# Kernel tuning notes

Hardware: AMD Instinct MI355X
Metric: run time of the kernel (lower is better)

Reference implementation:

```python
import jax, jax.numpy as jnp
import numpy as np

B, S, D = 2, 2048, 2048
H, KVH, HD = 8, 1, 256          # query heads, kv heads, head_dim (GQA: n_rep = H // KVH)
ROPE_THETA = 10000.0
NEG_INF = -1e9


def setup_inputs() -> dict:
    key = jax.random.key(0)
    k1, k2, k3, k4, k5 = jax.random.split(key, 5)
    hidden_states = jax.random.normal(k1, (B, S, D), dtype=jnp.float32)
    # additive causal mask: 0 where allowed, -inf where masked, shape (B,1,S,S)
    causal = jnp.tril(jnp.ones((S, S), dtype=bool))
    attention_mask = jnp.where(causal, 0.0, NEG_INF).astype(jnp.float32)
    attention_mask = jnp.broadcast_to(attention_mask[None, None], (B, 1, S, S))
    position_ids = jnp.broadcast_to(jnp.arange(S, dtype=jnp.int32)[None, :], (B, S))
    sc = 0.02
    Wq = jax.random.normal(k2, (H * HD, D), dtype=jnp.float32) * sc   # torch Linear weight layout [out,in]
    Wk = jax.random.normal(k3, (KVH * HD, D), dtype=jnp.float32) * sc
    Wv = jax.random.normal(k4, (KVH * HD, D), dtype=jnp.float32) * sc
    Wo = jax.random.normal(k5, (D, H * HD), dtype=jnp.float32) * sc
    return {"hidden_states": hidden_states, "attention_mask": attention_mask,
            "position_ids": position_ids, "Wq": Wq, "Wk": Wk, "Wv": Wv, "Wo": Wo}


def _rotate_half(x):
    x1, x2 = jnp.split(x, 2, axis=-1)
    return jnp.concatenate((-x2, x1), axis=-1)


def _rope_cos_sin(position_ids):
    inv_freq = 1.0 / (ROPE_THETA ** (jnp.arange(0, HD, 2, dtype=jnp.float32) / HD))  # [HD/2]
    freqs = position_ids.astype(jnp.float32)[:, :, None] * inv_freq[None, None, :]   # [B,S,HD/2]
    emb = jnp.concatenate((freqs, freqs), axis=-1)                                   # [B,S,HD]
    return jnp.cos(emb)[:, None], jnp.sin(emb)[:, None]                              # [B,1,S,HD]


def reference(hidden_states, attention_mask, position_ids, Wq, Wk, Wv, Wo):
    q = (hidden_states @ Wq.T).reshape(B, S, H, HD).transpose(0, 2, 1, 3)     # [B,H,S,HD]
    k = (hidden_states @ Wk.T).reshape(B, S, KVH, HD).transpose(0, 2, 1, 3)   # [B,KVH,S,HD]
    v = (hidden_states @ Wv.T).reshape(B, S, KVH, HD).transpose(0, 2, 1, 3)
    cos, sin = _rope_cos_sin(position_ids)
    q = q * cos + _rotate_half(q) * sin
    k = k * cos + _rotate_half(k) * sin
    n_rep = H // KVH
    k = jnp.repeat(k, n_rep, axis=1)                                          # repeat_kv -> [B,H,S,HD]
    v = jnp.repeat(v, n_rep, axis=1)
    scores = jnp.einsum('bhqd,bhkd->bhqk', q, k) / jnp.sqrt(jnp.float32(HD))
    scores = scores + attention_mask
    attn = jax.nn.softmax(scores, axis=-1)                                    # dropout p=0 (eval)
    ctx = jnp.einsum('bhqk,bhkd->bhqd', attn, v)
    ctx = ctx.transpose(0, 2, 1, 3).reshape(B, S, H * HD)
    out = ctx @ Wo.T
    return out, attn
```

## Files before the change

### kernel.cpp

```cpp
#include <hip/hip_runtime.h>
#include <hip/hip_bf16.h>
#include <math.h>

typedef __bf16 bf16_t;
typedef __bf16 bf16x8 __attribute__((ext_vector_type(8)));
typedef __bf16 bf16x4 __attribute__((ext_vector_type(4)));
typedef float  f32x4  __attribute__((ext_vector_type(4)));

#define DEV __device__ __forceinline__

constexpr int B_   = 2;
constexpr int S_   = 2048;
constexpr int D_   = 2048;
constexpr int H_   = 8;
constexpr int HD_  = 256;
constexpr int NQKV_ = H_ * HD_ + 2 * HD_;
constexpr int TOK_ = B_ * S_;

#if defined(__has_builtin)
#if __has_builtin(__builtin_amdgcn_global_load_lds)
#define HAS_GLLDS 1
#endif
#endif

DEV void stage16(const bf16_t* g, bf16_t* l) {
#ifdef HAS_GLLDS
  __builtin_amdgcn_global_load_lds((const __attribute__((address_space(1))) void*)g,
                                   (__attribute__((address_space(3))) void*)l, 16, 0, 0);
#else
  *(bf16x8*)l = *(const bf16x8*)g;
#endif
}

__global__ void cast_inputs(const float* __restrict__ hs, const float* __restrict__ wq,
                            const float* __restrict__ wk, const float* __restrict__ wv,
                            const float* __restrict__ wo,
                            bf16_t* __restrict__ Xb, bf16_t* __restrict__ Wqkvb,
                            bf16_t* __restrict__ Wob) {
  const size_t i = (size_t)blockIdx.x * blockDim.x + threadIdx.x;
  const size_t NHS = (size_t)TOK_ * D_;
  const size_t NWQ = (size_t)H_ * HD_ * D_;
  const size_t NWK = (size_t)HD_ * D_;
  if (i < NHS) Xb[i] = (bf16_t)hs[i];
  if (i < NWQ) { Wqkvb[i] = (bf16_t)wq[i]; Wob[i] = (bf16_t)wo[i]; }
  if (i < NWK) { Wqkvb[NWQ + i] = (bf16_t)wk[i]; Wqkvb[NWQ + NWK + i] = (bf16_t)wv[i]; }
}

template <int MODE>
__global__ __launch_bounds__(256, 2)
void gemm_bt(const void* __restrict__ Av, const bf16_t* __restrict__ Bg0,
             void* __restrict__ Cv,
             int M, int N, int K, int lda, int ldb, int ldc, float scale)
{
  const int bn = blockIdx.x, bm = blockIdx.y, z = blockIdx.z;
  if (MODE == 1 && bn > bm) return;

  const int m0 = bm * 128, n0 = bn * 128;
  const bf16_t* Ab = nullptr;
  const float*  Af = nullptr;
  const bf16_t* Bg = Bg0;
  if (MODE == 0) { Ab = (const bf16_t*)Av; }
  if (MODE == 1) { Ab = (const bf16_t*)Av + (size_t)z * S_ * HD_; Bg += (size_t)(z >> 3) * S_ * HD_; }
  if (MODE == 2) { Af = (const float*)Av + (size_t)z * S_ * S_;   Bg += (size_t)(z >> 3) * HD_ * S_; }

  int kend = K;
  if (MODE == 2) { int kl = (bm + 1) * 128; kend = kl < K ? kl : K; }

  __shared__ __align__(16) bf16_t Asm[128 * 32];
  __shared__ __align__(16) bf16_t Bsm[128 * 32];

  const int tid  = threadIdx.x;
  const int l    = tid & 63;
  const int w    = tid >> 6;
  const int wm   = (w >> 1) * 64;
  const int wn   = (w & 1) * 64;
  const int lrow = l & 15;
  const int quad = l >> 4;

  f32x4 acc[4][4] = {};

  for (int k0 = 0; k0 < kend; k0 += 32) {
    __syncthreads();
    if (MODE != 2) {
      #pragma unroll
      for (int c = 0; c < 2; ++c) {
        int chunk = c * 256 + tid;
        int row = chunk >> 2, col = (chunk & 3) << 3;
        stage16(Ab + (size_t)(m0 + row) * lda + (k0 + col), &Asm[row * 32 + col]);
      }
    } else {
      #pragma unroll
      for (int c = 0; c < 4; ++c) {
        int chunk = c * 256 + tid;
        int row = chunk >> 3, col = (chunk & 7) << 2;
        float4 v = *(const float4*)(Af + (size_t)(m0 + row) * lda + (k0 + col));
        bf16x4 t; t[0] = (bf16_t)v.x; t[1] = (bf16_t)v.y; t[2] = (bf16_t)v.z; t[3] = (bf16_t)v.w;
        *(bf16x4*)&Asm[row * 32 + col] = t;
      }
    }
    #pragma unroll
    for (int c = 0; c < 2; ++c) {
      int chunk = c * 256 + tid;
      int row = chunk >> 2, col = (chunk & 3) << 3;
      stage16(Bg + (size_t)(n0 + row) * ldb + (k0 + col), &Bsm[row * 32 + col]);
    }
    __syncthreads();

    bf16x8 af[4], bfr[4];
    #pragma unroll
    for (int i = 0; i < 4; ++i)
      af[i] = *(const bf16x8*)&Asm[(wm + i * 16 + lrow) * 32 + quad * 8];
    #pragma unroll
    for (int j = 0; j < 4; ++j)
      bfr[j] = *(const bf16x8*)&Bsm[(wn + j * 16 + lrow) * 32 + quad * 8];
    #pragma unroll
    for (int i = 0; i < 4; ++i)
      #pragma unroll
      for (int j = 0; j < 4; ++j)
        acc[i][j] = __builtin_amdgcn_mfma_f32_16x16x32_bf16(af[i], bfr[j], acc[i][j], 0, 0, 0);
  }

  if (MODE == 2) {
    bf16_t* C = (bf16_t*)Cv + (size_t)(z >> 3) * S_ * D_ + (size_t)(z & 7) * HD_;
    #pragma unroll
    for (int i = 0; i < 4; ++i) {
      int row = wm + i * 16 + quad * 4;
      #pragma unroll
      for (int j = 0; j < 4; ++j) {
        int col = n0 + wn + j * 16 + lrow;
        #pragma unroll
        for (int r = 0; r < 4; ++r)
          C[(size_t)(m0 + row + r) * ldc + col] = (bf16_t)(acc[i][j][r] * scale);
      }
    }
  } else {
    float* C = (float*)Cv;
    if (MODE == 1) C += (size_t)z * S_ * S_;
    #pragma unroll
    for (int i = 0; i < 4; ++i) {
      int row = wm + i * 16 + quad * 4;
      #pragma unroll
      for (int j = 0; j < 4; ++j) {
        int col = n0 + wn + j * 16 + lrow;
        #pragma unroll
        for (int r = 0; r < 4; ++r)
          C[(size_t)(m0 + row + r) * ldc + col] = acc[i][j][r] * scale;
      }
    }
  }
}

__global__ void rope_kernel(const float* __restrict__ qkv, const int* __restrict__ pos_ids,
                            bf16_t* __restrict__ Qh, bf16_t* __restrict__ Kb,
                            bf16_t* __restrict__ Vt)
{
  const int t = blockIdx.x;
  const int b = t >> 11, s = t & (S_ - 1);
  const int tid = threadIdx.x;
  const int pd = tid & 127, half = tid >> 7;
  const float pos = (float)pos_ids[t];
  const float expo = (float)(2 * pd) * (1.0f / 256.0f);
  const float invf = 1.0f / powf(10000.0f, expo);
  const float ang = pos * invf;
  const float c = cosf(ang), sn = sinf(ang);
  const float* base = qkv + (size_t)t * NQKV_;
  const int other = half ? tid - 128 : tid + 128;
  const float sgn = half ? 1.0f : -1.0f;
  #pragma unroll
  for (int h = 0; h < H_; ++h) {
    float x = base[h * HD_ + tid];
    float xo = base[h * HD_ + other];
    Qh[((size_t)(b * H_ + h) * S_ + s) * HD_ + tid] = (bf16_t)(x * c + sgn * xo * sn);
  }
  {
    float x = base[D_ + tid], xo = base[D_ + other];
    Kb[(size_t)t * HD_ + tid] = (bf16_t)(x * c + sgn * xo * sn);
  }
  {
    float x = base[D_ + HD_ + tid];
    Vt[((size_t)b * HD_ + tid) * S_ + s] = (bf16_t)x;
  }
}

__global__ __launch_bounds__(256)
void softmax_rows(float* __restrict__ attn)
{
  const int r = blockIdx.x;
  const int q = r & (S_ - 1);
  float* row = attn + (size_t)r * S_;
  const int tid = threadIdx.x;
  __shared__ float red[8];
  float vals[8];
  float mx = -3.0e38f;
  #pragma unroll
  for (int i = 0; i < 8; ++i) {
    int c = i * 256 + tid;
    float v = row[c];
    vals[i] = v;
    if (c <= q) mx = fmaxf(mx, v);
  }
  #pragma unroll
  for (int o = 32; o > 0; o >>= 1) mx = fmaxf(mx, __shfl_xor(mx, o, 64));
  if ((tid & 63) == 0) red[tid >> 6] = mx;
  __syncthreads();
  mx = fmaxf(fmaxf(red[0], red[1]), fmaxf(red[2], red[3]));
  float sum = 0.f;
  #pragma unroll
  for (int i = 0; i < 8; ++i) {
    int c = i * 256 + tid;
    if (c <= q) { vals[i] = __expf(vals[i] - mx); sum += vals[i]; }
    else vals[i] = 0.f;
  }
  #pragma unroll
  for (int o = 32; o > 0; o >>= 1) sum += __shfl_xor(sum, o, 64);
  if ((tid & 63) == 0) red[4 + (tid >> 6)] = sum;
  __syncthreads();
  sum = (red[4] + red[5]) + (red[6] + red[7]);
  const float inv = 1.0f / sum;
  #pragma unroll
  for (int i = 0; i < 8; ++i) {
    int c = i * 256 + tid;
    row[c] = vals[i] * inv;
  }
}

extern "C" void kernel_launch(void* const* d_in, const int* in_sizes, int n_in,
                              void* d_out, int out_size, void* d_ws, size_t ws_size,
                              hipStream_t stream)
{
  const float* hs  = (const float*)d_in[0];
  const int*   pos = (const int*)d_in[2];
  const float* wq  = (const float*)d_in[3];
  const float* wk  = (const float*)d_in[4];
  const float* wv  = (const float*)d_in[5];
  const float* wo  = (const float*)d_in[6];

  float* out  = (float*)d_out;
  float* attn = out + (size_t)TOK_ * D_;

  char* ws = (char*)d_ws;
  bf16_t* Xb    = (bf16_t*)(ws);
  bf16_t* Wqkvb = (bf16_t*)(ws + 16777216);
  bf16_t* Wob   = (bf16_t*)(ws + 27262976);
  float*  QKV   = (float* )(ws + 35651584);
  bf16_t* Ctx   = (bf16_t*)(ws + 35651584);
  bf16_t* Qh    = (bf16_t*)(ws + 77594624);
  bf16_t* Kb    = (bf16_t*)(ws + 94371840);
  bf16_t* Vt    = (bf16_t*)(ws + 96468992);

  cast_inputs<<<(TOK_ * D_) / 256, 256, 0, stream>>>(hs, wq, wk, wv, wo, Xb, Wqkvb, Wob);
  gemm_bt<0><<<dim3(NQKV_ / 128, TOK_ / 128, 1), 256, 0, stream>>>(
      Xb, Wqkvb, QKV, TOK_, NQKV_, D_, D_, D_, NQKV_, 1.0f);
  rope_kernel<<<TOK_, 256, 0, stream>>>(QKV, pos, Qh, Kb, Vt);
  gemm_bt<1><<<dim3(S_ / 128, S_ / 128, B_ * H_), 256, 0, stream>>>(
      Qh, Kb, attn, S_, S_, HD_, HD_, HD_, S_, 0.0625f);
  softmax_rows<<<B_ * H_ * S_, 256, 0, stream>>>(attn);
  gemm_bt<2><<<dim3(HD_ / 128, S_ / 128, B_ * H_), 256, 0, stream>>>(
      attn, Vt, Ctx, S_, HD_, S_, S_, S_, D_, 1.0f);
  gemm_bt<0><<<dim3(D_ / 128, TOK_ / 128, 1), 256, 0, stream>>>(
      Ctx, Wob, out, TOK_, D_, D_, D_, D_, D_, 1.0f);
}
```

Before: 678.5 us.

## Fuse QK^T, softmax and PV into a two-pass flash-attention kernel

Replaces the separate score GEMM, row softmax and PV GEMM with a single flash-attention kernel. A first pass computes running row max and sum, and a second pass recomputes the scores, writes normalized probabilities to attn (zeros above the diagonal), and accumulates P·V from a bf16 copy in shared memory. The goal is to avoid reading and rewriting the full fp32 attn matrix several times. The QKV projection now writes bf16 instead of fp32, which halves the intermediate traffic at some precision cost. QK^T is computed twice, and the per-element scattered fp32 stores of P may be poorly coalesced.

```diff
diff --git a/kernel.cpp b/kernel.cpp
--- a/kernel.cpp
+++ b/kernel.cpp
@@ -4,7 +4,6 @@
 
 typedef __bf16 bf16_t;
 typedef __bf16 bf16x8 __attribute__((ext_vector_type(8)));
-typedef __bf16 bf16x4 __attribute__((ext_vector_type(4)));
 typedef float  f32x4  __attribute__((ext_vector_type(4)));
 
 #define DEV __device__ __forceinline__
@@ -46,25 +45,13 @@
   if (i < NWK) { Wqkvb[NWQ + i] = (bf16_t)wk[i]; Wqkvb[NWQ + NWK + i] = (bf16_t)wv[i]; }
 }
 
-template <int MODE>
+template <bool CBF16>
 __global__ __launch_bounds__(256, 2)
-void gemm_bt(const void* __restrict__ Av, const bf16_t* __restrict__ Bg0,
-             void* __restrict__ Cv,
-             int M, int N, int K, int lda, int ldb, int ldc, float scale)
-{
-  const int bn = blockIdx.x, bm = blockIdx.y, z = blockIdx.z;
-  if (MODE == 1 && bn > bm) return;
-
+void gemm_bt(const bf16_t* __restrict__ Ab, const bf16_t* __restrict__ Bg,
+             void* __restrict__ Cv, int K, int lda, int ldb, int ldc)
+{
+  const int bn = blockIdx.x, bm = blockIdx.y;
   const int m0 = bm * 128, n0 = bn * 128;
-  const bf16_t* Ab = nullptr;
-  const float*  Af = nullptr;
-  const bf16_t* Bg = Bg0;
-  if (MODE == 0) { Ab = (const bf16_t*)Av; }
-  if (MODE == 1) { Ab = (const bf16_t*)Av + (size_t)z * S_ * HD_; Bg += (size_t)(z >> 3) * S_ * HD_; }
-  if (MODE == 2) { Af = (const float*)Av + (size_t)z * S_ * S_;   Bg += (size_t)(z >> 3) * HD_ * S_; }
-
-  int kend = K;
-  if (MODE == 2) { int kl = (bm + 1) * 128; kend = kl < K ? kl : K; }
 
   __shared__ __align__(16) bf16_t Asm[128 * 32];
   __shared__ __align__(16) bf16_t Bsm[128 * 32];
@@ -79,29 +66,13 @@
 
   f32x4 acc[4][4] = {};
 
-  for (int k0 = 0; k0 < kend; k0 += 32) {
+  for (int k0 = 0; k0 < K; k0 += 32) {
     __syncthreads();
-    if (MODE != 2) {
-      #pragma unroll
-      for (int c = 0; c < 2; ++c) {
-        int chunk = c * 256 + tid;
-        int row = chunk >> 2, col = (chunk & 3) << 3;
-        stage16(Ab + (size_t)(m0 + row) * lda + (k0 + col), &Asm[row * 32 + col]);
-      }
-    } else {
-      #pragma unroll
-      for (int c = 0; c < 4; ++c) {
-        int chunk = c * 256 + tid;
-        int row = chunk >> 3, col = (chunk & 7) << 2;
-        float4 v = *(const float4*)(Af + (size_t)(m0 + row) * lda + (k0 + col));
-        bf16x4 t; t[0] = (bf16_t)v.x; t[1] = (bf16_t)v.y; t[2] = (bf16_t)v.z; t[3] = (bf16_t)v.w;
-        *(bf16x4*)&Asm[row * 32 + col] = t;
-      }
-    }
     #pragma unroll
     for (int c = 0; c < 2; ++c) {
       int chunk = c * 256 + tid;
       int row = chunk >> 2, col = (chunk & 3) << 3;
+      stage16(Ab + (size_t)(m0 + row) * lda + (k0 + col), &Asm[row * 32 + col]);
       stage16(Bg + (size_t)(n0 + row) * ldb + (k0 + col), &Bsm[row * 32 + col]);
     }
     __syncthreads();
@@ -120,37 +91,22 @@
         acc[i][j] = __builtin_amdgcn_mfma_f32_16x16x32_bf16(af[i], bfr[j], acc[i][j], 0, 0, 0);
   }
 
-  if (MODE == 2) {
-    bf16_t* C = (bf16_t*)Cv + (size_t)(z >> 3) * S_ * D_ + (size_t)(z & 7) * HD_;
-    #pragma unroll
-    for (int i = 0; i < 4; ++i) {
-      int row = wm + i * 16 + quad * 4;
-      #pragma unroll
-      for (int j = 0; j < 4; ++j) {
-        int col = n0 + wn + j * 16 + lrow;
-        #pragma unroll
-        for (int r = 0; r < 4; ++r)
-          C[(size_t)(m0 + row + r) * ldc + col] = (bf16_t)(acc[i][j][r] * scale);
-      }
-    }
-  } else {
-    float* C = (float*)Cv;
-    if (MODE == 1) C += (size_t)z * S_ * S_;
-    #pragma unroll
-    for (int i = 0; i < 4; ++i) {
-      int row = wm + i * 16 + quad * 4;
-      #pragma unroll
-      for (int j = 0; j < 4; ++j) {
-        int col = n0 + wn + j * 16 + lrow;
-        #pragma unroll
-        for (int r = 0; r < 4; ++r)
-          C[(size_t)(m0 + row + r) * ldc + col] = acc[i][j][r] * scale;
-      }
-    }
-  }
-}
-
-__global__ void rope_kernel(const float* __restrict__ qkv, const int* __restrict__ pos_ids,
+  #pragma unroll
+  for (int i = 0; i < 4; ++i) {
+    int row = wm + i * 16 + quad * 4;
+    #pragma unroll
+    for (int j = 0; j < 4; ++j) {
+      int col = n0 + wn + j * 16 + lrow;
+      #pragma unroll
+      for (int r = 0; r < 4; ++r) {
+        if (CBF16) ((bf16_t*)Cv)[(size_t)(m0 + row + r) * ldc + col] = (bf16_t)acc[i][j][r];
+        else       ((float*) Cv)[(size_t)(m0 + row + r) * ldc + col] = acc[i][j][r];
+      }
+    }
+  }
+}
+
+__global__ void rope_kernel(const bf16_t* __restrict__ qkv, const int* __restrict__ pos_ids,
                             bf16_t* __restrict__ Qh, bf16_t* __restrict__ Kb,
                             bf16_t* __restrict__ Vt)
 {
@@ -163,64 +119,177 @@
   const float invf = 1.0f / powf(10000.0f, expo);
   const float ang = pos * invf;
   const float c = cosf(ang), sn = sinf(ang);
-  const float* base = qkv + (size_t)t * NQKV_;
+  const bf16_t* base = qkv + (size_t)t * NQKV_;
   const int other = half ? tid - 128 : tid + 128;
   const float sgn = half ? 1.0f : -1.0f;
   #pragma unroll
   for (int h = 0; h < H_; ++h) {
-    float x = base[h * HD_ + tid];
-    float xo = base[h * HD_ + other];
+    float x = (float)base[h * HD_ + tid];
+    float xo = (float)base[h * HD_ + other];
     Qh[((size_t)(b * H_ + h) * S_ + s) * HD_ + tid] = (bf16_t)(x * c + sgn * xo * sn);
   }
   {
-    float x = base[D_ + tid], xo = base[D_ + other];
+    float x = (float)base[D_ + tid], xo = (float)base[D_ + other];
     Kb[(size_t)t * HD_ + tid] = (bf16_t)(x * c + sgn * xo * sn);
   }
-  {
-    float x = base[D_ + HD_ + tid];
-    Vt[((size_t)b * HD_ + tid) * S_ + s] = (bf16_t)x;
-  }
-}
-
-__global__ __launch_bounds__(256)
-void softmax_rows(float* __restrict__ attn)
-{
-  const int r = blockIdx.x;
-  const int q = r & (S_ - 1);
-  float* row = attn + (size_t)r * S_;
+  Vt[((size_t)b * HD_ + tid) * S_ + s] = base[D_ + HD_ + tid];
+}
+
+constexpr int PSTR = 136;
+
+DEV void compute_S(const bf16_t* __restrict__ Kg, bf16_t* __restrict__ KV,
+                   const bf16x8 aq[8], f32x4 accS[8],
+                   int kb, int tid, int lrow, int quad)
+{
+  #pragma unroll
+  for (int half = 0; half < 2; ++half) {
+    __syncthreads();
+    #pragma unroll
+    for (int it = 0; it < 8; ++it) {
+      int s = it * 256 + tid;
+      int c = s >> 6, key = s & 63;
+      stage16(Kg + (size_t)(kb * 128 + half * 64 + key) * HD_ + c * 8, KV + s * 8);
+    }
+    __syncthreads();
+    #pragma unroll
+    for (int kk = 0; kk < 8; ++kk) {
+      bf16x8 bk[4];
+      #pragma unroll
+      for (int j = 0; j < 4; ++j)
+        bk[j] = *(const bf16x8*)&KV[((kk * 4 + quad) * 64 + j * 16 + lrow) * 8];
+      #pragma unroll
+      for (int j = 0; j < 4; ++j)
+        accS[half * 4 + j] =
+            __builtin_amdgcn_mfma_f32_16x16x32_bf16(aq[kk], bk[j], accS[half * 4 + j], 0, 0, 0);
+    }
+  }
+}
+
+__global__ __launch_bounds__(256, 2)
+void flash_attn(const bf16_t* __restrict__ Qh, const bf16_t* __restrict__ Kbp,
+                const bf16_t* __restrict__ Vt, float* __restrict__ attn,
+                bf16_t* __restrict__ Ctx)
+{
+  const int z = blockIdx.x;
+  const int qb = blockIdx.y;
+  const int b = z >> 3, h = z & 7;
+  const int q0 = qb * 64;
+  const bf16_t* Qg = Qh + ((size_t)z * S_ + q0) * HD_;
+  const bf16_t* Kg = Kbp + (size_t)b * S_ * HD_;
+  const bf16_t* Vg = Vt + (size_t)b * HD_ * S_;
+  float* Pg = attn + (size_t)z * S_ * S_ + (size_t)q0 * S_;
+
+  __shared__ __align__(16) bf16_t KV[64 * 256];
+  __shared__ __align__(16) bf16_t Pst[4 * 16 * PSTR];
+
   const int tid = threadIdx.x;
-  __shared__ float red[8];
-  float vals[8];
-  float mx = -3.0e38f;
-  #pragma unroll
-  for (int i = 0; i < 8; ++i) {
-    int c = i * 256 + tid;
-    float v = row[c];
-    vals[i] = v;
-    if (c <= q) mx = fmaxf(mx, v);
-  }
-  #pragma unroll
-  for (int o = 32; o > 0; o >>= 1) mx = fmaxf(mx, __shfl_xor(mx, o, 64));
-  if ((tid & 63) == 0) red[tid >> 6] = mx;
-  __syncthreads();
-  mx = fmaxf(fmaxf(red[0], red[1]), fmaxf(red[2], red[3]));
-  float sum = 0.f;
-  #pragma unroll
-  for (int i = 0; i < 8; ++i) {
-    int c = i * 256 + tid;
-    if (c <= q) { vals[i] = __expf(vals[i] - mx); sum += vals[i]; }
-    else vals[i] = 0.f;
-  }
-  #pragma unroll
-  for (int o = 32; o > 0; o >>= 1) sum += __shfl_xor(sum, o, 64);
-  if ((tid & 63) == 0) red[4 + (tid >> 6)] = sum;
-  __syncthreads();
-  sum = (red[4] + red[5]) + (red[6] + red[7]);
-  const float inv = 1.0f / sum;
-  #pragma unroll
-  for (int i = 0; i < 8; ++i) {
-    int c = i * 256 + tid;
-    row[c] = vals[i] * inv;
+  const int w = tid >> 6, l = tid & 63;
+  const int lrow = l & 15, quad = l >> 4;
+  const int nkb = (qb >> 1) + 1;
+  const float scale = 0.0625f;
+
+  for (int kb = nkb; kb < S_ / 128; ++kb) {
+    #pragma unroll
+    for (int it = 0; it < 8; ++it) {
+      int idx = it * 256 + tid;
+      int row = idx >> 5, c4 = idx & 31;
+      *(f32x4*)&Pg[(size_t)row * S_ + kb * 128 + c4 * 4] = f32x4{0.f, 0.f, 0.f, 0.f};
+    }
+  }
+
+  bf16x8 aq[8];
+  const bf16_t* qrow = Qg + (size_t)(w * 16 + lrow) * HD_ + quad * 8;
+  #pragma unroll
+  for (int kk = 0; kk < 8; ++kk) aq[kk] = *(const bf16x8*)(qrow + kk * 32);
+
+  float m[4], lsum[4];
+  #pragma unroll
+  for (int r = 0; r < 4; ++r) { m[r] = -3.0e38f; lsum[r] = 0.f; }
+
+  const int rowg0 = q0 + w * 16 + quad * 4;
+
+  for (int kb = 0; kb < nkb; ++kb) {
+    f32x4 accS[8] = {};
+    compute_S(Kg, KV, aq, accS, kb, tid, lrow, quad);
+    #pragma unroll
+    for (int r = 0; r < 4; ++r) {
+      float sv[8], tmax = -3.0e38f;
+      #pragma unroll
+      for (int j = 0; j < 8; ++j) {
+        float s = accS[j][r] * scale;
+        int col = kb * 128 + j * 16 + lrow;
+        if (col > rowg0 + r) s = -3.0e38f;
+        sv[j] = s;
+        tmax = fmaxf(tmax, s);
+      }
+      #pragma unroll
+      for (int o = 1; o < 16; o <<= 1) tmax = fmaxf(tmax, __shfl_xor(tmax, o, 64));
+      float mn = fmaxf(m[r], tmax);
+      float add = 0.f;
+      #pragma unroll
+      for (int j = 0; j < 8; ++j) add += __expf(sv[j] - mn);
+      #pragma unroll
+      for (int o = 1; o < 16; o <<= 1) add += __shfl_xor(add, o, 64);
+      lsum[r] = lsum[r] * __expf(m[r] - mn) + add;
+      m[r] = mn;
+    }
+  }
+
+  float mp[4];
+  #pragma unroll
+  for (int r = 0; r < 4; ++r) mp[r] = m[r] + __logf(lsum[r]);
+
+  f32x4 accO[16] = {};
+  bf16_t* pw = &Pst[w * 16 * PSTR];
+
+  for (int kb = 0; kb < nkb; ++kb) {
+    f32x4 accS[8] = {};
+    compute_S(Kg, KV, aq, accS, kb, tid, lrow, quad);
+
+    #pragma unroll
+    for (int r = 0; r < 4; ++r) {
+      float* prow = Pg + (size_t)(w * 16 + quad * 4 + r) * S_ + kb * 128;
+      #pragma unroll
+      for (int j = 0; j < 8; ++j) {
+        int col = kb * 128 + j * 16 + lrow;
+        float p = (col <= rowg0 + r) ? __expf(accS[j][r] * scale - mp[r]) : 0.f;
+        prow[j * 16 + lrow] = p;
+        pw[(quad * 4 + r) * PSTR + j * 16 + lrow] = (bf16_t)p;
+      }
+    }
+    bf16x8 ap[4];
+    #pragma unroll
+    for (int kk2 = 0; kk2 < 4; ++kk2)
+      ap[kk2] = *(const bf16x8*)&pw[lrow * PSTR + kk2 * 32 + quad * 8];
+
+    #pragma unroll
+    for (int half = 0; half < 2; ++half) {
+      __syncthreads();
+      #pragma unroll
+      for (int it = 0; it < 8; ++it) {
+        int s = it * 256 + tid;
+        int c2 = s >> 8, d = s & 255;
+        stage16(Vg + (size_t)d * S_ + kb * 128 + half * 64 + c2 * 8, KV + s * 8);
+      }
+      __syncthreads();
+      #pragma unroll
+      for (int kkl = 0; kkl < 2; ++kkl) {
+        #pragma unroll
+        for (int j2 = 0; j2 < 16; ++j2) {
+          bf16x8 bv = *(const bf16x8*)&KV[((kkl * 4 + quad) * 256 + j2 * 16 + lrow) * 8];
+          accO[j2] = __builtin_amdgcn_mfma_f32_16x16x32_bf16(ap[half * 2 + kkl], bv, accO[j2], 0, 0, 0);
+        }
+      }
+    }
+  }
+
+  #pragma unroll
+  for (int j2 = 0; j2 < 16; ++j2) {
+    #pragma unroll
+    for (int r = 0; r < 4; ++r) {
+      int rowq = q0 + w * 16 + quad * 4 + r;
+      Ctx[((size_t)b * S_ + rowq) * D_ + h * HD_ + j2 * 16 + lrow] = (bf16_t)accO[j2][r];
+    }
   }
 }
 
@@ -242,21 +311,17 @@
   bf16_t* Xb    = (bf16_t*)(ws);
   bf16_t* Wqkvb = (bf16_t*)(ws + 16777216);
   bf16_t* Wob   = (bf16_t*)(ws + 27262976);
-  float*  QKV   = (float* )(ws + 35651584);
-  bf16_t* Ctx   = (bf16_t*)(ws + 35651584);
-  bf16_t* Qh    = (bf16_t*)(ws + 77594624);
-  bf16_t* Kb    = (bf16_t*)(ws + 94371840);
-  bf16_t* Vt    = (bf16_t*)(ws + 96468992);
+  bf16_t* QKVb  = (bf16_t*)(ws + 35651584);
+  bf16_t* Qh    = (bf16_t*)(ws + 56623104);
+  bf16_t* Kb    = (bf16_t*)(ws + 73400320);
+  bf16_t* Vt    = (bf16_t*)(ws + 75497472);
+  bf16_t* Ctx   = (bf16_t*)(ws + 77594624);
 
   cast_inputs<<<(TOK_ * D_) / 256, 256, 0, stream>>>(hs, wq, wk, wv, wo, Xb, Wqkvb, Wob);
-  gemm_bt<0><<<dim3(NQKV_ / 128, TOK_ / 128, 1), 256, 0, stream>>>(
-      Xb, Wqkvb, QKV, TOK_, NQKV_, D_, D_, D_, NQKV_, 1.0f);
-  rope_kernel<<<TOK_, 256, 0, stream>>>(QKV, pos, Qh, Kb, Vt);
-  gemm_bt<1><<<dim3(S_ / 128, S_ / 128, B_ * H_), 256, 0, stream>>>(
-      Qh, Kb, attn, S_, S_, HD_, HD_, HD_, S_, 0.0625f);
-  softmax_rows<<<B_ * H_ * S_, 256, 0, stream>>>(attn);
-  gemm_bt<2><<<dim3(HD_ / 128, S_ / 128, B_ * H_), 256, 0, stream>>>(
-      attn, Vt, Ctx, S_, HD_, S_, S_, S_, D_, 1.0f);
-  gemm_bt<0><<<dim3(D_ / 128, TOK_ / 128, 1), 256, 0, stream>>>(
-      Ctx, Wob, out, TOK_, D_, D_, D_, D_, D_, 1.0f);
-}
+  gemm_bt<true><<<dim3(NQKV_ / 128, TOK_ / 128), 256, 0, stream>>>(
+      Xb, Wqkvb, QKVb, D_, D_, D_, NQKV_);
+  rope_kernel<<<TOK_, 256, 0, stream>>>(QKVb, pos, Qh, Kb, Vt);
+  flash_attn<<<dim3(B_ * H_, S_ / 64), 256, 0, stream>>>(Qh, Kb, Vt, attn, Ctx);
+  gemm_bt<false><<<dim3(D_ / 128, TOK_ / 128), 256, 0, stream>>>(
+      Ctx, Wob, out, D_, D_, D_, D_);
+}
```

Measured after the change: 667.5 us. No clear change (-1.6%).
